# Performance work log

Measured on AMD Instinct MI355X. Metric: run time of the kernel, lower is better.

## Reference

```python
import jax, jax.numpy as jnp
import numpy as np

N_EMBD = 2048
N_HEAD = 16
HEAD_DIM = N_EMBD // N_HEAD
MAX_SEQ = 2048
ROPE_BASE = 10000.0


def _build_rope_cache(seq_len, head_dim, base):
    theta = 1.0 / (base ** (jnp.arange(0, head_dim, 2, dtype=jnp.float32) / head_dim))
    idx_theta = jnp.arange(seq_len, dtype=jnp.float32)[:, None] * theta[None, :]  # [T, hd/2]
    return jnp.cos(idx_theta), jnp.sin(idx_theta)


def _apply_rope(x, cos, sin):
    # x: [B, T, H, hd]; interleaved (even, odd) pairing along last dim
    B, T, H, hd = x.shape
    xf = x.astype(jnp.float32).reshape(B, T, H, hd // 2, 2)
    x0, x1 = xf[..., 0], xf[..., 1]
    c = cos[None, :T, None, :]
    s = sin[None, :T, None, :]
    out = jnp.stack([x0 * c - x1 * s, x1 * c + x0 * s], axis=-1)
    return out.reshape(B, T, H, hd).astype(x.dtype)


def setup_inputs() -> dict:
    key = jax.random.key(0)
    k1, k2, k3 = jax.random.split(key, 3)
    x = jax.random.normal(k1, (2, 2048, N_EMBD), dtype=jnp.float32)
    # torch Linear(D, 3D, bias=False): y = x @ W.T ; store as [D, 3D] for x @ W
    scale = 1.0 / np.sqrt(N_EMBD)
    w_attn = jax.random.normal(k2, (N_EMBD, 3 * N_EMBD), dtype=jnp.float32) * scale
    w_proj = jax.random.normal(k3, (N_EMBD, N_EMBD), dtype=jnp.float32) * scale
    return {"x": x, "w_attn": w_attn, "w_proj": w_proj}


def reference(x, w_attn, w_proj):
    B, T, D = x.shape
    cos, sin = _build_rope_cache(MAX_SEQ, HEAD_DIM, ROPE_BASE)
    qkv = x @ w_attn                                   # [B, T, 3D]
    q, k, v = jnp.split(qkv, 3, axis=-1)
    q = q.reshape(B, T, N_HEAD, HEAD_DIM)
    k = k.reshape(B, T, N_HEAD, HEAD_DIM)
    v = v.reshape(B, T, N_HEAD, HEAD_DIM)
    q = _apply_rope(q, cos, sin)
    k = _apply_rope(k, cos, sin)
    # non-causal SDPA (original calls F.sdpa without is_causal)
    scale = 1.0 / jnp.sqrt(jnp.asarray(HEAD_DIM, dtype=q.dtype))
    scores = jnp.einsum("bqhd,bkhd->bhqk", q, k) * scale
    attn = jax.nn.softmax(scores, axis=-1)
    y = jnp.einsum("bhqk,bkhd->bqhd", attn, v).reshape(B, T, D)
    return y @ w_proj
```

## Files before the change

kernel.cpp:

```cpp
#include <hip/hip_runtime.h>
#include <cstdint>
#include <cstddef>

typedef __attribute__((ext_vector_type(8))) short bf16x8;
typedef __attribute__((ext_vector_type(8))) unsigned short us8;
typedef __attribute__((ext_vector_type(4))) float f32x4;

#define TSEQ 2048

__device__ __forceinline__ unsigned short f2bf(float f) {
  union { float f; uint32_t u; } v; v.f = f;
  uint32_t u = v.u;
  uint32_t r = (u + 0x7FFFu + ((u >> 16) & 1u)) >> 16;
  return (unsigned short)r;
}
__device__ __forceinline__ unsigned short f2bf_trunc(float f) {
  union { float f; uint32_t u; } v; v.f = f;
  return (unsigned short)(v.u >> 16);
}
__device__ __forceinline__ float bf2f(unsigned short h) {
  union { uint32_t u; float f; } v; v.u = ((uint32_t)h) << 16;
  return v.f;
}

__device__ __forceinline__ void async16(const void* g, void* l) {
  __builtin_amdgcn_global_load_lds(
      (const __attribute__((address_space(1))) unsigned int*)g,
      (__attribute__((address_space(3))) unsigned int*)l,
      16, 0, 0);
}

__global__ __launch_bounds__(256) void cvt_x(
    const float* __restrict__ in, unsigned short* __restrict__ out)
{
  const size_t i = ((size_t)blockIdx.x * 256 + threadIdx.x) * 16;
  f32x4 a0 = *(const f32x4*)(in + i);
  f32x4 a1 = *(const f32x4*)(in + i + 4);
  f32x4 a2 = *(const f32x4*)(in + i + 8);
  f32x4 a3 = *(const f32x4*)(in + i + 12);
  us8 lo, hi;
#pragma unroll
  for (int j = 0; j < 4; j++) {
    lo[j] = f2bf(a0[j]); lo[j + 4] = f2bf(a1[j]);
    hi[j] = f2bf(a2[j]); hi[j + 4] = f2bf(a3[j]);
  }
  *(us8*)(out + i) = lo;
  *(us8*)(out + i + 8) = hi;
}

__global__ __launch_bounds__(256) void transpose_w(
    const float* __restrict__ in, unsigned short* __restrict__ out,
    int R, int C)
{
  __shared__ unsigned short tile[32][33];
  const int bx = blockIdx.x * 32;
  const int by = blockIdx.y * 32;
  const int tx = threadIdx.x & 31;
  const int ty = threadIdx.x >> 5;
#pragma unroll
  for (int r = ty; r < 32; r += 8)
    tile[r][tx] = f2bf(in[(size_t)(by + r) * C + bx + tx]);
  __syncthreads();
#pragma unroll
  for (int r = ty; r < 32; r += 8)
    out[(size_t)(bx + r) * R + by + tx] = tile[tx][r];
}

template <int CF32>
__global__ __launch_bounds__(256) void gemm_bt(
    const unsigned short* __restrict__ A,
    const unsigned short* __restrict__ Bt,
    void* __restrict__ Cv,
    int M, int N, int K, int ldc)
{
  __shared__ unsigned short As[2][128 * 32];
  __shared__ unsigned short Bs[2][128 * 32];
  const int tid  = threadIdx.x;
  const int lane = tid & 63;
  const int w    = tid >> 6;
  const int m0   = blockIdx.y * 128;
  const int n0   = blockIdx.x * 128;
  const int wm   = (w & 1) * 64;
  const int wn   = (w >> 1) * 64;

  const int srow = lane >> 2;
  const int scol = (lane & 3) * 8;
  const unsigned short* ga0 = A  + (size_t)(m0 + w * 16 + srow) * K + scol;
  const unsigned short* ga1 = ga0 + (size_t)64 * K;
  const unsigned short* gb0 = Bt + (size_t)(n0 + w * 16 + srow) * K + scol;
  const unsigned short* gb1 = gb0 + (size_t)64 * K;

  f32x4 acc[4][4];
#pragma unroll
  for (int i = 0; i < 4; i++)
#pragma unroll
    for (int j = 0; j < 4; j++) acc[i][j] = (f32x4){0.f, 0.f, 0.f, 0.f};

  const int frow = lane & 15;
  const int fcol = (lane >> 4) * 8;

  for (int kt = 0; kt < K; kt += 64) {
    __syncthreads();
    async16(ga0 + kt,      &As[0][w * 512]);
    async16(ga1 + kt,      &As[0][(4 + w) * 512]);
    async16(ga0 + kt + 32, &As[1][w * 512]);
    async16(ga1 + kt + 32, &As[1][(4 + w) * 512]);
    async16(gb0 + kt,      &Bs[0][w * 512]);
    async16(gb1 + kt,      &Bs[0][(4 + w) * 512]);
    async16(gb0 + kt + 32, &Bs[1][w * 512]);
    async16(gb1 + kt + 32, &Bs[1][(4 + w) * 512]);
    __syncthreads();

#pragma unroll
    for (int h = 0; h < 2; h++) {
      bf16x8 af[4], bfr[4];
#pragma unroll
      for (int i = 0; i < 4; i++)
        af[i] = *(const bf16x8*)&As[h][(wm + i * 16 + frow) * 32 + fcol];
#pragma unroll
      for (int i = 0; i < 4; i++)
        bfr[i] = *(const bf16x8*)&Bs[h][(wn + i * 16 + frow) * 32 + fcol];
#pragma unroll
      for (int mi = 0; mi < 4; mi++)
#pragma unroll
        for (int ni = 0; ni < 4; ni++)
          acc[mi][ni] = __builtin_amdgcn_mfma_f32_16x16x32_bf16(
              af[mi], bfr[ni], acc[mi][ni], 0, 0, 0);
    }
  }

  const int crow0 = m0 + wm + (lane >> 4) * 4;
  const int ccol0 = n0 + wn + (lane & 15);
  if (CF32) {
    float* Cf = (float*)Cv;
#pragma unroll
    for (int mi = 0; mi < 4; mi++)
#pragma unroll
      for (int i = 0; i < 4; i++) {
        const int row = crow0 + mi * 16 + i;
#pragma unroll
        for (int ni = 0; ni < 4; ni++)
          Cf[(size_t)row * ldc + ccol0 + ni * 16] = acc[mi][ni][i];
      }
  } else {
    unsigned short* Cb = (unsigned short*)Cv;
#pragma unroll
    for (int mi = 0; mi < 4; mi++)
#pragma unroll
      for (int i = 0; i < 4; i++) {
        const int row = crow0 + mi * 16 + i;
#pragma unroll
        for (int ni = 0; ni < 4; ni++)
          Cb[(size_t)row * ldc + ccol0 + ni * 16] = f2bf(acc[mi][ni][i]);
      }
  }
}

__global__ __launch_bounds__(256) void rope_qk(unsigned short* __restrict__ qkv)
{
  const int q   = blockIdx.x * 256 + threadIdx.x;
  const int row = q >> 9;
  const int cb  = (q & 511) * 8;
  const int t   = row & (TSEQ - 1);
  const int hd  = cb & 127;
  const float sc = (cb < 2048) ? 0.08838834764831845f : 1.0f;
  unsigned short* base = qkv + (size_t)row * 6144 + cb;
  uint4 u = *(const uint4*)base;
  uint32_t wd[4] = {u.x, u.y, u.z, u.w};
#pragma unroll
  for (int k = 0; k < 4; k++) {
    const float theta = exp2f((float)(hd + 2 * k) * -0.1038102531f);
    float s, c;
    sincosf((float)t * theta, &s, &c);
    const float x0 = bf2f((unsigned short)(wd[k] & 0xffffu));
    const float x1 = bf2f((unsigned short)(wd[k] >> 16));
    const float o0 = (x0 * c - x1 * s) * sc;
    const float o1 = (x1 * c + x0 * s) * sc;
    wd[k] = (uint32_t)f2bf(o0) | ((uint32_t)f2bf(o1) << 16);
  }
  *(uint4*)base = make_uint4(wd[0], wd[1], wd[2], wd[3]);
}

__global__ __launch_bounds__(256) void repack_v(
    const unsigned short* __restrict__ qkv, unsigned short* __restrict__ Vtg)
{
  __shared__ unsigned short tile[128][72];
  const int tt = blockIdx.x * 64;
  const int bh = blockIdx.y;
  const int b  = bh >> 4, h = bh & 15;

  {
    const int r  = threadIdx.x & 63;
    const int i0 = threadIdx.x >> 6;
    const unsigned short* src =
        qkv + (size_t)(b * TSEQ + tt + r) * 6144 + 4096 + h * 128;
#pragma unroll
    for (int i = i0; i < 16; i += 4) {
      us8 v = *(const us8*)(src + i * 8);
#pragma unroll
      for (int k = 0; k < 8; k++) tile[i * 8 + k][r] = v[k];
    }
  }
  __syncthreads();
  {
    unsigned short* dst = Vtg + (size_t)bh * 262144 + tt;
#pragma unroll
    for (int it = 0; it < 4; it++) {
      const int wdx = it * 256 + threadIdx.x;
      const int d = wdx >> 3;
      const int j = (wdx & 7) * 8;
      us8 v = *(const us8*)&tile[d][j];
      *(us8*)(dst + (size_t)d * TSEQ + j) = v;
    }
  }
}

__global__ __launch_bounds__(256) void attn(
    const unsigned short* __restrict__ qkv,
    const unsigned short* __restrict__ Vtg,
    unsigned short* __restrict__ y)
{
  __shared__ unsigned short Ks[64 * 136];
  __shared__ unsigned short Vs[128 * 72];
  __shared__ unsigned short Ps[4][32 * 72];

  const int tid  = threadIdx.x;
  const int lane = tid & 63;
  const int w    = tid >> 6;
  const int q0   = blockIdx.x * 128;
  const int h    = blockIdx.y;
  const int b    = blockIdx.z;
  const int bh   = b * 16 + h;
  const int quad = lane >> 4;
  const int l15  = lane & 15;
  const int kq   = quad * 8;

  bf16x8 qa[2][4];
#pragma unroll
  for (int mt = 0; mt < 2; mt++) {
    const unsigned short* gQ =
        qkv + (size_t)(b * TSEQ + q0 + w * 32 + mt * 16 + l15) * 6144 + h * 128 + kq;
#pragma unroll
    for (int dc = 0; dc < 4; dc++) qa[mt][dc] = *(const bf16x8*)(gQ + dc * 32);
  }

  f32x4 ot[2][8];
#pragma unroll
  for (int mt = 0; mt < 2; mt++)
#pragma unroll
    for (int nt = 0; nt < 8; nt++) ot[mt][nt] = (f32x4){0.f, 0.f, 0.f, 0.f};
  float rs[2][4];
#pragma unroll
  for (int mt = 0; mt < 2; mt++)
#pragma unroll
    for (int i = 0; i < 4; i++) rs[mt][i] = 0.f;

  const int krow = tid >> 2;
  const int kd   = (tid & 3) * 32;
  const unsigned short* gK = qkv + (size_t)(b * TSEQ) * 6144 + 2048 + h * 128 + kd;
  const int vd = tid >> 1;
  const int vc = (tid & 1) * 32;
  const unsigned short* gVt = Vtg + (size_t)bh * 262144 + (size_t)vd * TSEQ + vc;

  us8 kreg[4], vreg[4];
  {
    const unsigned short* pk = gK + (size_t)krow * 6144;
#pragma unroll
    for (int j = 0; j < 4; j++) kreg[j] = *(const us8*)(pk + j * 8);
#pragma unroll
    for (int j = 0; j < 4; j++) vreg[j] = *(const us8*)(gVt + j * 8);
  }

  for (int kb = 0; kb < TSEQ; kb += 64) {
    __syncthreads();
#pragma unroll
    for (int j = 0; j < 4; j++)
      *(us8*)&Ks[krow * 136 + kd + j * 8] = kreg[j];
#pragma unroll
    for (int j = 0; j < 4; j++)
      *(us8*)&Vs[vd * 72 + vc + j * 8] = vreg[j];
    __syncthreads();

    if (kb + 64 < TSEQ) {
      const unsigned short* pk = gK + (size_t)(kb + 64 + krow) * 6144;
#pragma unroll
      for (int j = 0; j < 4; j++) kreg[j] = *(const us8*)(pk + j * 8);
      const unsigned short* pv = gVt + kb + 64;
#pragma unroll
      for (int j = 0; j < 4; j++) vreg[j] = *(const us8*)(pv + j * 8);
    }

    f32x4 s[2][4];
#pragma unroll
    for (int mt = 0; mt < 2; mt++)
#pragma unroll
      for (int ct = 0; ct < 4; ct++) s[mt][ct] = (f32x4){0.f, 0.f, 0.f, 0.f};
    __builtin_amdgcn_s_setprio(1);
#pragma unroll
    for (int dc = 0; dc < 4; dc++) {
#pragma unroll
      for (int ct = 0; ct < 4; ct++) {
        bf16x8 kf = *(const bf16x8*)&Ks[(ct * 16 + l15) * 136 + dc * 32 + kq];
        s[0][ct] = __builtin_amdgcn_mfma_f32_16x16x32_bf16(qa[0][dc], kf, s[0][ct], 0, 0, 0);
        s[1][ct] = __builtin_amdgcn_mfma_f32_16x16x32_bf16(qa[1][dc], kf, s[1][ct], 0, 0, 0);
      }
    }
    __builtin_amdgcn_s_setprio(0);

    unsigned short* pw = &Ps[w][0];
    float t8[2][4];
#pragma unroll
    for (int mt = 0; mt < 2; mt++)
#pragma unroll
      for (int i = 0; i < 4; i++) t8[mt][i] = 0.f;
#pragma unroll
    for (int mt = 0; mt < 2; mt++)
#pragma unroll
      for (int ct = 0; ct < 4; ct++)
#pragma unroll
        for (int i = 0; i < 4; i++) {
          const unsigned short us = f2bf_trunc(__expf(fminf(s[mt][ct][i], 30.f)));
          pw[(mt * 16 + quad * 4 + i) * 72 + ct * 16 + l15] = us;
          t8[mt][i] += bf2f(us);
        }
#pragma unroll
    for (int mt = 0; mt < 2; mt++)
#pragma unroll
      for (int i = 0; i < 4; i++) {
        float v = t8[mt][i];
        v += __shfl_xor(v, 1);
        v += __shfl_xor(v, 2);
        v += __shfl_xor(v, 4);
        v += __shfl_xor(v, 8);
        rs[mt][i] += v;
      }

    __asm__ volatile("s_waitcnt lgkmcnt(0)" ::: "memory");

    __builtin_amdgcn_s_setprio(1);
#pragma unroll
    for (int kc = 0; kc < 2; kc++) {
      bf16x8 pa0 = *(const bf16x8*)&pw[(l15) * 72 + kc * 32 + kq];
      bf16x8 pa1 = *(const bf16x8*)&pw[(16 + l15) * 72 + kc * 32 + kq];
#pragma unroll
      for (int nt = 0; nt < 8; nt++) {
        bf16x8 vb = *(const bf16x8*)&Vs[(nt * 16 + l15) * 72 + kc * 32 + kq];
        ot[0][nt] = __builtin_amdgcn_mfma_f32_16x16x32_bf16(pa0, vb, ot[0][nt], 0, 0, 0);
        ot[1][nt] = __builtin_amdgcn_mfma_f32_16x16x32_bf16(pa1, vb, ot[1][nt], 0, 0, 0);
      }
    }
    __builtin_amdgcn_s_setprio(0);
  }

#pragma unroll
  for (int mt = 0; mt < 2; mt++) {
    unsigned short* gy =
        y + (size_t)(b * TSEQ + q0 + w * 32 + mt * 16 + quad * 4) * 2048 + h * 128 + l15;
#pragma unroll
    for (int i = 0; i < 4; i++) {
      const float inv = 1.0f / rs[mt][i];
#pragma unroll
      for (int nt = 0; nt < 8; nt++)
        gy[(size_t)i * 2048 + nt * 16] = f2bf(ot[mt][nt][i] * inv);
    }
  }
}

extern "C" void kernel_launch(void* const* d_in, const int* in_sizes, int n_in,
                              void* d_out, int out_size, void* d_ws, size_t ws_size,
                              hipStream_t stream)
{
  const float* x      = (const float*)d_in[0];
  const float* w_attn = (const float*)d_in[1];
  const float* w_proj = (const float*)d_in[2];

  if (ws_size < 67108864u) return;

  char* ws = (char*)d_ws;
  unsigned short* qkv = (unsigned short*)(ws);
  unsigned short* xb  = (unsigned short*)(ws + 50331648);
  unsigned short* y   = xb;
  unsigned short* wT2 = (unsigned short*)(ws);
  unsigned short* wTa = (unsigned short*)d_out;
  unsigned short* Vtg = (unsigned short*)d_out;

  transpose_w<<<dim3(192, 64), 256, 0, stream>>>(w_attn, wTa, 2048, 6144);
  cvt_x<<<dim3(2048), 256, 0, stream>>>(x, xb);
  gemm_bt<0><<<dim3(48, 32), 256, 0, stream>>>(xb, wTa, (void*)qkv, 4096, 6144, 2048, 6144);
  rope_qk<<<dim3(8192), 256, 0, stream>>>(qkv);
  repack_v<<<dim3(32, 32), 256, 0, stream>>>(qkv, Vtg);
  attn<<<dim3(16, 16, 2), 256, 0, stream>>>(qkv, Vtg, y);
  transpose_w<<<dim3(64, 64), 256, 0, stream>>>(w_proj, wT2, 2048, 2048);
  gemm_bt<1><<<dim3(16, 32), 256, 0, stream>>>(y, wT2, d_out, 4096, 2048, 2048, 2048);
}
```

Baseline: 430.9 us.

## Double-buffer K/V register prefetch, defer row-sum reduction, remap attention grid

The attention kernel now keeps two register sets of K/V tiles and alternates them, so prefetch loads go two tiles ahead instead of one. The per-tile cross-lane shuffle reduction of the softmax row sum is replaced by a per-lane accumulation that is reduced once at the end. The grid is flattened to 1D with a swizzled mapping that groups 8 heads per query block to improve L2 reuse of K/V. The costs are higher register pressure from the extra prefetch buffers, which may reduce occupancy, and a slightly different summation order.

```diff
diff --git a/kernel.cpp b/kernel.cpp
--- a/kernel.cpp
+++ b/kernel.cpp
@@ -227,10 +227,11 @@
   const int tid  = threadIdx.x;
   const int lane = tid & 63;
   const int w    = tid >> 6;
-  const int q0   = blockIdx.x * 128;
-  const int h    = blockIdx.y;
-  const int b    = blockIdx.z;
-  const int bh   = b * 16 + h;
+  const int d    = blockIdx.x;
+  const int bh   = ((d >> 7) << 3) | (d & 7);
+  const int q0   = ((d >> 3) & 15) * 128;
+  const int b    = bh >> 4;
+  const int h    = bh & 15;
   const int quad = lane >> 4;
   const int l15  = lane & 15;
   const int kq   = quad * 8;
@@ -262,95 +263,81 @@
   const int vc = (tid & 1) * 32;
   const unsigned short* gVt = Vtg + (size_t)bh * 262144 + (size_t)vd * TSEQ + vc;
 
-  us8 kreg[4], vreg[4];
+  us8 kX[4], vX[4], kY[4], vY[4];
   {
     const unsigned short* pk = gK + (size_t)krow * 6144;
 #pragma unroll
-    for (int j = 0; j < 4; j++) kreg[j] = *(const us8*)(pk + j * 8);
-#pragma unroll
-    for (int j = 0; j < 4; j++) vreg[j] = *(const us8*)(gVt + j * 8);
-  }
-
-  for (int kb = 0; kb < TSEQ; kb += 64) {
-    __syncthreads();
-#pragma unroll
-    for (int j = 0; j < 4; j++)
-      *(us8*)&Ks[krow * 136 + kd + j * 8] = kreg[j];
-#pragma unroll
-    for (int j = 0; j < 4; j++)
-      *(us8*)&Vs[vd * 72 + vc + j * 8] = vreg[j];
-    __syncthreads();
-
-    if (kb + 64 < TSEQ) {
-      const unsigned short* pk = gK + (size_t)(kb + 64 + krow) * 6144;
-#pragma unroll
-      for (int j = 0; j < 4; j++) kreg[j] = *(const us8*)(pk + j * 8);
-      const unsigned short* pv = gVt + kb + 64;
-#pragma unroll
-      for (int j = 0; j < 4; j++) vreg[j] = *(const us8*)(pv + j * 8);
-    }
-
-    f32x4 s[2][4];
-#pragma unroll
-    for (int mt = 0; mt < 2; mt++)
-#pragma unroll
-      for (int ct = 0; ct < 4; ct++) s[mt][ct] = (f32x4){0.f, 0.f, 0.f, 0.f};
-    __builtin_amdgcn_s_setprio(1);
-#pragma unroll
-    for (int dc = 0; dc < 4; dc++) {
-#pragma unroll
-      for (int ct = 0; ct < 4; ct++) {
-        bf16x8 kf = *(const bf16x8*)&Ks[(ct * 16 + l15) * 136 + dc * 32 + kq];
-        s[0][ct] = __builtin_amdgcn_mfma_f32_16x16x32_bf16(qa[0][dc], kf, s[0][ct], 0, 0, 0);
-        s[1][ct] = __builtin_amdgcn_mfma_f32_16x16x32_bf16(qa[1][dc], kf, s[1][ct], 0, 0, 0);
-      }
-    }
-    __builtin_amdgcn_s_setprio(0);
-
-    unsigned short* pw = &Ps[w][0];
-    float t8[2][4];
-#pragma unroll
-    for (int mt = 0; mt < 2; mt++)
-#pragma unroll
-      for (int i = 0; i < 4; i++) t8[mt][i] = 0.f;
-#pragma unroll
-    for (int mt = 0; mt < 2; mt++)
-#pragma unroll
-      for (int ct = 0; ct < 4; ct++)
-#pragma unroll
-        for (int i = 0; i < 4; i++) {
-          const unsigned short us = f2bf_trunc(__expf(fminf(s[mt][ct][i], 30.f)));
-          pw[(mt * 16 + quad * 4 + i) * 72 + ct * 16 + l15] = us;
-          t8[mt][i] += bf2f(us);
-        }
-#pragma unroll
-    for (int mt = 0; mt < 2; mt++)
-#pragma unroll
-      for (int i = 0; i < 4; i++) {
-        float v = t8[mt][i];
-        v += __shfl_xor(v, 1);
-        v += __shfl_xor(v, 2);
-        v += __shfl_xor(v, 4);
-        v += __shfl_xor(v, 8);
-        rs[mt][i] += v;
-      }
-
-    __asm__ volatile("s_waitcnt lgkmcnt(0)" ::: "memory");
-
-    __builtin_amdgcn_s_setprio(1);
-#pragma unroll
-    for (int kc = 0; kc < 2; kc++) {
-      bf16x8 pa0 = *(const bf16x8*)&pw[(l15) * 72 + kc * 32 + kq];
-      bf16x8 pa1 = *(const bf16x8*)&pw[(16 + l15) * 72 + kc * 32 + kq];
-#pragma unroll
-      for (int nt = 0; nt < 8; nt++) {
-        bf16x8 vb = *(const bf16x8*)&Vs[(nt * 16 + l15) * 72 + kc * 32 + kq];
-        ot[0][nt] = __builtin_amdgcn_mfma_f32_16x16x32_bf16(pa0, vb, ot[0][nt], 0, 0, 0);
-        ot[1][nt] = __builtin_amdgcn_mfma_f32_16x16x32_bf16(pa1, vb, ot[1][nt], 0, 0, 0);
-      }
-    }
-    __builtin_amdgcn_s_setprio(0);
-  }
+    for (int j = 0; j < 4; j++) kX[j] = *(const us8*)(pk + j * 8);
+#pragma unroll
+    for (int j = 0; j < 4; j++) vX[j] = *(const us8*)(gVt + j * 8);
+    const unsigned short* pk2 = gK + (size_t)(64 + krow) * 6144;
+#pragma unroll
+    for (int j = 0; j < 4; j++) kY[j] = *(const us8*)(pk2 + j * 8);
+#pragma unroll
+    for (int j = 0; j < 4; j++) vY[j] = *(const us8*)(gVt + 64 + j * 8);
+  }
+
+#define HALF_STEP(KR, VR, pfc, pfoff)                                          \
+  do {                                                                         \
+    __syncthreads();                                                           \
+    _Pragma("unroll") for (int j = 0; j < 4; j++)                              \
+        *(us8*)&Ks[krow * 136 + kd + j * 8] = KR[j];                           \
+    _Pragma("unroll") for (int j = 0; j < 4; j++)                              \
+        *(us8*)&Vs[vd * 72 + vc + j * 8] = VR[j];                              \
+    __syncthreads();                                                           \
+    if (pfc) {                                                                 \
+      const unsigned short* pk = gK + (size_t)((pfoff) + krow) * 6144;         \
+      _Pragma("unroll") for (int j = 0; j < 4; j++)                            \
+          KR[j] = *(const us8*)(pk + j * 8);                                   \
+      const unsigned short* pv = gVt + (pfoff);                                \
+      _Pragma("unroll") for (int j = 0; j < 4; j++)                            \
+          VR[j] = *(const us8*)(pv + j * 8);                                   \
+    }                                                                          \
+    f32x4 s[2][4];                                                             \
+    _Pragma("unroll") for (int mt = 0; mt < 2; mt++)                           \
+      _Pragma("unroll") for (int ct = 0; ct < 4; ct++)                         \
+          s[mt][ct] = (f32x4){0.f, 0.f, 0.f, 0.f};                             \
+    __builtin_amdgcn_s_setprio(1);                                             \
+    _Pragma("unroll") for (int dc = 0; dc < 4; dc++) {                         \
+      _Pragma("unroll") for (int ct = 0; ct < 4; ct++) {                       \
+        bf16x8 kf = *(const bf16x8*)&Ks[(ct * 16 + l15) * 136 + dc * 32 + kq]; \
+        s[0][ct] = __builtin_amdgcn_mfma_f32_16x16x32_bf16(                    \
+            qa[0][dc], kf, s[0][ct], 0, 0, 0);                                 \
+        s[1][ct] = __builtin_amdgcn_mfma_f32_16x16x32_bf16(                    \
+            qa[1][dc], kf, s[1][ct], 0, 0, 0);                                 \
+      }                                                                        \
+    }                                                                          \
+    __builtin_amdgcn_s_setprio(0);                                             \
+    unsigned short* pw = &Ps[w][0];                                            \
+    _Pragma("unroll") for (int mt = 0; mt < 2; mt++)                           \
+      _Pragma("unroll") for (int ct = 0; ct < 4; ct++)                         \
+        _Pragma("unroll") for (int i = 0; i < 4; i++) {                        \
+          const unsigned short us =                                            \
+              f2bf_trunc(__expf(fminf(s[mt][ct][i], 30.f)));                   \
+          pw[(mt * 16 + quad * 4 + i) * 72 + ct * 16 + l15] = us;              \
+          rs[mt][i] += bf2f(us);                                               \
+        }                                                                      \
+    __asm__ volatile("s_waitcnt lgkmcnt(0)" ::: "memory");                     \
+    __builtin_amdgcn_s_setprio(1);                                             \
+    _Pragma("unroll") for (int kc = 0; kc < 2; kc++) {                         \
+      bf16x8 pa0 = *(const bf16x8*)&pw[(l15) * 72 + kc * 32 + kq];             \
+      bf16x8 pa1 = *(const bf16x8*)&pw[(16 + l15) * 72 + kc * 32 + kq];        \
+      _Pragma("unroll") for (int nt = 0; nt < 8; nt++) {                       \
+        bf16x8 vb = *(const bf16x8*)&Vs[(nt * 16 + l15) * 72 + kc * 32 + kq];  \
+        ot[0][nt] = __builtin_amdgcn_mfma_f32_16x16x32_bf16(                   \
+            pa0, vb, ot[0][nt], 0, 0, 0);                                      \
+        ot[1][nt] = __builtin_amdgcn_mfma_f32_16x16x32_bf16(                   \
+            pa1, vb, ot[1][nt], 0, 0, 0);                                      \
+      }                                                                        \
+    }                                                                          \
+    __builtin_amdgcn_s_setprio(0);                                             \
+  } while (0)
+
+  for (int kb = 0; kb < TSEQ; kb += 128) {
+    HALF_STEP(kX, vX, kb + 128 < TSEQ, kb + 128);
+    HALF_STEP(kY, vY, kb + 192 < TSEQ, kb + 192);
+  }
+#undef HALF_STEP
 
 #pragma unroll
   for (int mt = 0; mt < 2; mt++) {
@@ -358,7 +345,12 @@
         y + (size_t)(b * TSEQ + q0 + w * 32 + mt * 16 + quad * 4) * 2048 + h * 128 + l15;
 #pragma unroll
     for (int i = 0; i < 4; i++) {
-      const float inv = 1.0f / rs[mt][i];
+      float v = rs[mt][i];
+      v += __shfl_xor(v, 1);
+      v += __shfl_xor(v, 2);
+      v += __shfl_xor(v, 4);
+      v += __shfl_xor(v, 8);
+      const float inv = 1.0f / v;
 #pragma unroll
       for (int nt = 0; nt < 8; nt++)
         gy[(size_t)i * 2048 + nt * 16] = f2bf(ot[mt][nt][i] * inv);
@@ -389,7 +381,7 @@
   gemm_bt<0><<<dim3(48, 32), 256, 0, stream>>>(xb, wTa, (void*)qkv, 4096, 6144, 2048, 6144);
   rope_qk<<<dim3(8192), 256, 0, stream>>>(qkv);
   repack_v<<<dim3(32, 32), 256, 0, stream>>>(qkv, Vtg);
-  attn<<<dim3(16, 16, 2), 256, 0, stream>>>(qkv, Vtg, y);
+  attn<<<dim3(512), 256, 0, stream>>>(qkv, Vtg, y);
   transpose_w<<<dim3(64, 64), 256, 0, stream>>>(w_proj, wT2, 2048, 2048);
   gemm_bt<1><<<dim3(16, 32), 256, 0, stream>>>(y, wT2, d_out, 4096, 2048, 2048, 2048);
 }
```

After: 449.9 us. 4.4% more time.
